# Kernel tuning notes

Measured on AMD Instinct MI355X. Metric: run time of the kernel, lower is better.

Reference implementation:

```python
import jax, jax.numpy as jnp
import numpy as np

SEQ_LEN = 2048
DIM = 1024
DIM_HEAD = 64
NHEAD = DIM // DIM_HEAD


def setup_inputs() -> dict:
    key = jax.random.key(0)
    k1, k2, k3 = jax.random.split(key, 3)
    x = jax.random.normal(k1, (SEQ_LEN, DIM), dtype=jnp.float32)
    # ortho_init approximated by scaled gaussian weights (same math path in forward)
    Wqkv = jax.random.normal(k2, (DIM, 3 * DIM), dtype=jnp.float32) / np.sqrt(DIM)
    Wout = jax.random.normal(k3, (DIM, DIM), dtype=jnp.float32) / np.sqrt(DIM)
    bias = jnp.zeros((DIM,), dtype=jnp.float32)
    return {"x": x, "Wqkv": Wqkv, "Wout": Wout, "bias": bias}


def reference(x, Wqkv, Wout, bias):
    seq_len = x.shape[-2]
    qkv = x @ Wqkv  # [S, 3*dim]
    qkv = jnp.reshape(qkv, (-1, 3, NHEAD, DIM_HEAD))  # [S,3,H,D]
    qkv = jnp.swapaxes(qkv, 0, 2)  # [H,3,S,D]
    q, k, v = (jax.lax.index_in_dim(qkv, i, -3, keepdims=False) for i in range(3))
    # [H,S,S] full logits, scaled
    logits = q @ jnp.swapaxes(k, -1, -2) / jnp.sqrt(DIM_HEAD)
    mask = jnp.tril(jnp.ones((seq_len, seq_len), dtype=jnp.float32))
    logits = jnp.where(mask, logits, jnp.finfo(logits.dtype).min)
    dtype = logits.dtype
    probs = jax.nn.softmax(logits.astype(jnp.float32), axis=-1).astype(dtype)
    attn_outs = probs @ v  # [H,S,D]
    attn_outs = jnp.reshape(jnp.swapaxes(attn_outs, 0, 1), (-1, NHEAD * DIM_HEAD))
    return attn_outs @ Wout + bias
```

## Files before the change

kernel.cpp:

```cpp
#include <hip/hip_runtime.h>
#include <cstdint>

#define SEQ_LEN 2048
#define DIM 1024
#define NHEAD 16
#define DHEAD 64
#define QKV_LD (3 * DIM)

typedef unsigned short u16;
typedef short bf16x8 __attribute__((ext_vector_type(8)));
typedef float f32x4 __attribute__((ext_vector_type(4)));

__device__ __forceinline__ u16 f2bf(float f) {
    union { float f; unsigned u; } v;
    v.f = f;
    unsigned r = v.u + 0x7fff + ((v.u >> 16) & 1);
    return (u16)(r >> 16);
}

__device__ __forceinline__ void load_lds16(const void* g, void* l) {
    __builtin_amdgcn_global_load_lds(
        (const __attribute__((address_space(1))) void*)g,
        (__attribute__((address_space(3))) void*)l, 16, 0, 0);
}

__device__ __forceinline__ void transpose_tile(const float* __restrict__ W,
                                               u16* __restrict__ Wt, int K, int N,
                                               int bx, int by, int t, float (*tile)[33]) {
    const int n0 = bx * 32, k0 = by * 32;
    const int tx = t & 31, ty = t >> 5;
#pragma unroll
    for (int i = 0; i < 32; i += 8)
        tile[ty + i][tx] = W[(size_t)(k0 + ty + i) * N + n0 + tx];
    __syncthreads();
#pragma unroll
    for (int i = 0; i < 32; i += 8)
        Wt[(size_t)(n0 + ty + i) * K + k0 + tx] = f2bf(tile[tx][ty + i]);
}

__global__ __launch_bounds__(256) void prep_k(const float* __restrict__ x,
                                              const float* __restrict__ Wqkv,
                                              const float* __restrict__ Wout,
                                              u16* __restrict__ xb,
                                              u16* __restrict__ Wqkvt,
                                              u16* __restrict__ Woutt) {
    __shared__ float tile[32][33];
    const int b = blockIdx.x;
    const int t = threadIdx.x;
    if (b < 2048) {
        const int i = b * 256 + t;
        const float4 v = reinterpret_cast<const float4*>(x)[i];
        const unsigned p0 = (unsigned)f2bf(v.x) | ((unsigned)f2bf(v.y) << 16);
        const unsigned p1 = (unsigned)f2bf(v.z) | ((unsigned)f2bf(v.w) << 16);
        reinterpret_cast<uint2*>(xb)[i] = make_uint2(p0, p1);
    } else if (b < 5120) {
        const int b2 = b - 2048;
        transpose_tile(Wqkv, Wqkvt, DIM, QKV_LD, b2 % 96, b2 / 96, t, tile);
    } else {
        const int b3 = b - 5120;
        transpose_tile(Wout, Woutt, DIM, DIM, b3 & 31, b3 >> 5, t, tile);
    }
}

template <int MODE, int BM, int BN, int BK>
__global__ __launch_bounds__(256) void gemm_bf16(const u16* __restrict__ A,
                                                 const u16* __restrict__ Bt,
                                                 const float* __restrict__ bias,
                                                 void* __restrict__ Cout,
                                                 int M, int N, int K) {
    constexpr int AI = BM / 32;
    constexpr int BJ = BN / 32;
    constexpr int ASZ = BM * BK;
    constexpr int BSZ = BN * BK;
    __shared__ u16 As[2 * ASZ];
    __shared__ u16 Bs[2 * BSZ];

    const int t = threadIdx.x;
    const int lane = t & 63;
    const int quad = lane >> 4;
    const int l15 = lane & 15;
    const int w = t >> 6;
    const int wm = (w & 1) * (BM / 2);
    const int wn = (w >> 1) * (BN / 2);
    const int m0 = blockIdx.y * BM;
    const int n0 = blockIdx.x * BN;
    const int sr = t >> 2;
    const int sc = (t & 3) << 3;

    const u16* Ab = A + (size_t)(m0 + sr) * K + sc;
    const u16* Bb = Bt + (size_t)(n0 + sr) * K + sc;

    auto stage = [&](int buf, int k0) {
#pragma unroll
        for (int kc = 0; kc < BK / 32; ++kc) {
#pragma unroll
            for (int c = 0; c < BM / 64; ++c)
                load_lds16(Ab + (size_t)(c * 64) * K + k0 + kc * 32,
                           &As[buf * ASZ + kc * BM * 32 + c * 2048 + t * 8]);
#pragma unroll
            for (int c = 0; c < BN / 64; ++c)
                load_lds16(Bb + (size_t)(c * 64) * K + k0 + kc * 32,
                           &Bs[buf * BSZ + kc * BN * 32 + c * 2048 + t * 8]);
        }
    };

    stage(0, 0);
    f32x4 acc[AI][BJ] = {};

    const int niter = K / BK;
    for (int it = 0; it < niter; ++it) {
        const int cur = it & 1, nxt = cur ^ 1;
        __syncthreads();
        if (it + 1 < niter) stage(nxt, (it + 1) * BK);
#pragma unroll
        for (int kc = 0; kc < BK / 32; ++kc) {
            bf16x8 af[AI], bfr[BJ];
#pragma unroll
            for (int i = 0; i < AI; ++i)
                af[i] = *reinterpret_cast<const bf16x8*>(
                    &As[cur * ASZ + kc * BM * 32 + (wm + i * 16 + l15) * 32 + quad * 8]);
#pragma unroll
            for (int j = 0; j < BJ; ++j)
                bfr[j] = *reinterpret_cast<const bf16x8*>(
                    &Bs[cur * BSZ + kc * BN * 32 + (wn + j * 16 + l15) * 32 + quad * 8]);
#pragma unroll
            for (int i = 0; i < AI; ++i)
#pragma unroll
                for (int j = 0; j < BJ; ++j)
                    acc[i][j] =
                        __builtin_amdgcn_mfma_f32_16x16x32_bf16(af[i], bfr[j], acc[i][j], 0, 0, 0);
        }
    }

#pragma unroll
    for (int j = 0; j < BJ; ++j) {
        const int col = n0 + wn + j * 16 + l15;
        float bv = 0.f;
        if constexpr (MODE == 1) bv = bias[col];
#pragma unroll
        for (int i = 0; i < AI; ++i) {
            const int row = m0 + wm + i * 16 + quad * 4;
#pragma unroll
            for (int r = 0; r < 4; ++r) {
                const float v = acc[i][j][r];
                if constexpr (MODE == 1)
                    ((float*)Cout)[(size_t)(row + r) * N + col] = v + bv;
                else
                    ((u16*)Cout)[(size_t)(row + r) * N + col] = f2bf(v);
            }
        }
    }
}

__global__ __launch_bounds__(256) void attn_mfma(const u16* __restrict__ qkv,
                                                 u16* __restrict__ O) {
    constexpr int PSTR = 40;
    __shared__ u16 SM[2560 + 4096 + 4096];
    u16* Ps = SM;
    u16* Ks = SM + 2560;
    u16* Vt = SM + 2560 + 4096;
    float* Ored = (float*)SM;
    float* Lred = Ored + 32 * 66;

    const int b = blockIdx.x;
    const int i = 63 - (b >> 4);
    const int h = b & 15;
    const int q0 = i * 32;
    const int jmax = i >> 1;

    const int t = threadIdx.x;
    const int lane = t & 63;
    const int quad = lane >> 4;
    const int l15 = lane & 15;
    const int w = t >> 6;
    const int wq = w >> 1;
    const int wk = w & 1;

    const int sr = t >> 2;
    const int sc = (t & 3) << 3;
    const int vp = (t & 31) * 2;
    const int vq = (t >> 5) * 8;

    load_lds16(qkv + (size_t)(q0 + ((t >> 2) & 31)) * QKV_LD + h * DHEAD + (t >> 7) * 32 + sc,
               &SM[t * 8]);
    const u16* kp0 = qkv + (size_t)sr * QKV_LD + DIM + h * DHEAD + sc;
    uint4 ka = *reinterpret_cast<const uint4*>(kp0);
    uint4 kb = *reinterpret_cast<const uint4*>(kp0 + 32);
    const u16* vp0 = qkv + (size_t)vp * QKV_LD + 2 * DIM + h * DHEAD + vq;
    uint4 va = *reinterpret_cast<const uint4*>(vp0);
    uint4 vb = *reinterpret_cast<const uint4*>(vp0 + QKV_LD);

    __syncthreads();
    const bf16x8 qf0 = *reinterpret_cast<const bf16x8*>(&SM[(wq * 16 + l15) * 32 + quad * 8]);
    const bf16x8 qf1 =
        *reinterpret_cast<const bf16x8*>(&SM[1024 + (wq * 16 + l15) * 32 + quad * 8]);
    __syncthreads();

    auto writeKV = [&](const uint4& kA, const uint4& kB, const uint4& vA, const uint4& vB) {
        *reinterpret_cast<uint4*>(&Ks[t * 8]) = kA;
        *reinterpret_cast<uint4*>(&Ks[2048 + t * 8]) = kB;
        const unsigned a4[4] = {vA.x, vA.y, vA.z, vA.w};
        const unsigned b4[4] = {vB.x, vB.y, vB.z, vB.w};
#pragma unroll
        for (int idx = 0; idx < 8; ++idx) {
            const unsigned lo = (idx & 1) ? (a4[idx >> 1] >> 16) : (a4[idx >> 1] & 0xffffu);
            const unsigned hi = (idx & 1) ? (b4[idx >> 1] >> 16) : (b4[idx >> 1] & 0xffffu);
            const int d = vq + idx;
            const int pos = d * 64 + (((vp >> 3) ^ (d & 7)) << 3) + (vp & 7);
            *reinterpret_cast<unsigned*>(&Vt[pos]) = lo | (hi << 16);
        }
    };
    writeKV(ka, kb, va, vb);
    __syncthreads();

    f32x4 oacc[4] = {};
    float lsum[4] = {0.f, 0.f, 0.f, 0.f};
    u16* Pw = Ps + w * 16 * PSTR;
    const int rowl_base = (i & 1) * 32 + wq * 16 + quad * 4;
    constexpr float SCL = 0.18033688f;

    for (int jt = 0; jt <= jmax; ++jt) {
        if (jt < jmax) {
            const int j1 = (jt + 1) * 64;
            const u16* kp = qkv + (size_t)(j1 + sr) * QKV_LD + DIM + h * DHEAD + sc;
            ka = *reinterpret_cast<const uint4*>(kp);
            kb = *reinterpret_cast<const uint4*>(kp + 32);
            const u16* vpt = qkv + (size_t)(j1 + vp) * QKV_LD + 2 * DIM + h * DHEAD + vq;
            va = *reinterpret_cast<const uint4*>(vpt);
            vb = *reinterpret_cast<const uint4*>(vpt + QKV_LD);
        }

        f32x4 sacc[2] = {};
#pragma unroll
        for (int nn = 0; nn < 2; ++nn) {
            const int krow = (wk * 32 + nn * 16 + l15) * 32 + quad * 8;
            const bf16x8 kf0 = *reinterpret_cast<const bf16x8*>(&Ks[krow]);
            sacc[nn] = __builtin_amdgcn_mfma_f32_16x16x32_bf16(qf0, kf0, sacc[nn], 0, 0, 0);
            const bf16x8 kf1 = *reinterpret_cast<const bf16x8*>(&Ks[2048 + krow]);
            sacc[nn] = __builtin_amdgcn_mfma_f32_16x16x32_bf16(qf1, kf1, sacc[nn], 0, 0, 0);
        }

        const bool diag = (jt == jmax);
#pragma unroll
        for (int r = 0; r < 4; ++r) {
            float p0 = sacc[0][r] * SCL, p1 = sacc[1][r] * SCL;
            if (diag) {
                const int rowl = rowl_base + r;
                if (wk * 32 + l15 > rowl) p0 = -1e30f;
                if (wk * 32 + 16 + l15 > rowl) p1 = -1e30f;
            }
            p0 = exp2f(p0);
            p1 = exp2f(p1);
            lsum[r] += p0 + p1;
            Pw[(quad * 4 + r) * PSTR + l15] = (u16)(__float_as_uint(p0) >> 16);
            Pw[(quad * 4 + r) * PSTR + 16 + l15] = (u16)(__float_as_uint(p1) >> 16);
        }

        const bf16x8 pf = *reinterpret_cast<const bf16x8*>(&Pw[l15 * PSTR + quad * 8]);
#pragma unroll
        for (int nd = 0; nd < 4; ++nd) {
            const int dloc = nd * 16 + l15;
            const bf16x8 vf = *reinterpret_cast<const bf16x8*>(
                &Vt[dloc * 64 + (((wk * 4 + quad) ^ (dloc & 7)) << 3)]);
            oacc[nd] = __builtin_amdgcn_mfma_f32_16x16x32_bf16(pf, vf, oacc[nd], 0, 0, 0);
        }

        if (jt < jmax) {
            __syncthreads();
            writeKV(ka, kb, va, vb);
            __syncthreads();
        }
    }

#pragma unroll
    for (int r = 0; r < 4; ++r) {
        float l = lsum[r];
#pragma unroll
        for (int off = 1; off < 16; off <<= 1) l += __shfl_xor(l, off, 64);
        lsum[r] = l;
    }
    __syncthreads();
    if (l15 == 0)
#pragma unroll
        for (int r = 0; r < 4; ++r) Lred[wk * 32 + wq * 16 + quad * 4 + r] = lsum[r];
    if (wk == 1)
#pragma unroll
        for (int nd = 0; nd < 4; ++nd)
#pragma unroll
            for (int r = 0; r < 4; ++r)
                Ored[(wq * 16 + quad * 4 + r) * 66 + nd * 16 + l15] = oacc[nd][r];
    __syncthreads();
    if (wk == 0) {
        float inv[4];
#pragma unroll
        for (int r = 0; r < 4; ++r) {
            const int rr = wq * 16 + quad * 4 + r;
            inv[r] = 1.0f / (Lred[rr] + Lred[32 + rr]);
        }
#pragma unroll
        for (int nd = 0; nd < 4; ++nd)
#pragma unroll
            for (int r = 0; r < 4; ++r) {
                const int rr = wq * 16 + quad * 4 + r;
                O[(size_t)(q0 + rr) * DIM + h * DHEAD + nd * 16 + l15] =
                    f2bf((oacc[nd][r] + Ored[rr * 66 + nd * 16 + l15]) * inv[r]);
            }
    }
}

extern "C" void kernel_launch(void* const* d_in, const int* in_sizes, int n_in,
                              void* d_out, int out_size, void* d_ws, size_t ws_size,
                              hipStream_t stream) {
    const float* x = (const float*)d_in[0];
    const float* Wqkv = (const float*)d_in[1];
    const float* Wout = (const float*)d_in[2];
    const float* bias = (const float*)d_in[3];
    float* out = (float*)d_out;

    char* ws = (char*)d_ws;
    u16* xb = (u16*)ws;
    u16* Wqkvt = (u16*)(ws + (4u << 20));
    u16* Woutt = (u16*)(ws + (10u << 20));
    u16* qkvb = (u16*)(ws + (12u << 20));
    u16* Ob = (u16*)(ws + (24u << 20));

    prep_k<<<dim3(6144), 256, 0, stream>>>(x, Wqkv, Wout, xb, Wqkvt, Woutt);

    gemm_bf16<0, 128, 64, 32><<<dim3(QKV_LD / 64, SEQ_LEN / 128), 256, 0, stream>>>(
        xb, Wqkvt, nullptr, qkvb, SEQ_LEN, QKV_LD, DIM);

    attn_mfma<<<dim3(64 * NHEAD), 256, 0, stream>>>(qkvb, Ob);

    gemm_bf16<1, 64, 64, 64><<<dim3(DIM / 64, SEQ_LEN / 64), 256, 0, stream>>>(
        Ob, Woutt, bias, out, SEQ_LEN, DIM, DIM);
}
```

Measured before the change: 151.6 us.

## Split causal attention over key chunks with a separate partial-sum reduction kernel

The single attention kernel becomes two kernels. The first processes at most four 64-key tiles per block, spread over a second grid dimension, and writes unnormalized fp32 partial outputs and row sums to workspace. The second kernel adds up the chunks, normalizes, and writes the bf16 output. This is meant to remove the causal load imbalance, where late query tiles looped over up to 32 key tiles, and to expose more parallel blocks. The cost is extra fp32 partial traffic to global memory, one more launch, and many blocks that exit early.

```diff
diff --git a/kernel.cpp b/kernel.cpp
--- a/kernel.cpp
+++ b/kernel.cpp
@@ -152,8 +152,9 @@
     }
 }
 
-__global__ __launch_bounds__(256) void attn_mfma(const u16* __restrict__ qkv,
-                                                 u16* __restrict__ O) {
+__global__ __launch_bounds__(256) void attn_part(const u16* __restrict__ qkv,
+                                                 float* __restrict__ Opart,
+                                                 float* __restrict__ Lpart) {
     constexpr int PSTR = 40;
     __shared__ u16 SM[2560 + 4096 + 4096];
     u16* Ps = SM;
@@ -162,11 +163,15 @@
     float* Ored = (float*)SM;
     float* Lred = Ored + 32 * 66;
 
-    const int b = blockIdx.x;
-    const int i = 63 - (b >> 4);
-    const int h = b & 15;
+    const int ih = blockIdx.x;
+    const int i = ih >> 4;
+    const int h = ih & 15;
+    const int c = blockIdx.y;
+    if (c > (i >> 3)) return;
     const int q0 = i * 32;
     const int jmax = i >> 1;
+    const int jlo = c * 4;
+    const int jhi = min(jlo + 3, jmax);
 
     const int t = threadIdx.x;
     const int lane = t & 63;
@@ -183,10 +188,10 @@
 
     load_lds16(qkv + (size_t)(q0 + ((t >> 2) & 31)) * QKV_LD + h * DHEAD + (t >> 7) * 32 + sc,
                &SM[t * 8]);
-    const u16* kp0 = qkv + (size_t)sr * QKV_LD + DIM + h * DHEAD + sc;
+    const u16* kp0 = qkv + (size_t)(jlo * 64 + sr) * QKV_LD + DIM + h * DHEAD + sc;
     uint4 ka = *reinterpret_cast<const uint4*>(kp0);
     uint4 kb = *reinterpret_cast<const uint4*>(kp0 + 32);
-    const u16* vp0 = qkv + (size_t)vp * QKV_LD + 2 * DIM + h * DHEAD + vq;
+    const u16* vp0 = qkv + (size_t)(jlo * 64 + vp) * QKV_LD + 2 * DIM + h * DHEAD + vq;
     uint4 va = *reinterpret_cast<const uint4*>(vp0);
     uint4 vb = *reinterpret_cast<const uint4*>(vp0 + QKV_LD);
 
@@ -219,8 +224,8 @@
     const int rowl_base = (i & 1) * 32 + wq * 16 + quad * 4;
     constexpr float SCL = 0.18033688f;
 
-    for (int jt = 0; jt <= jmax; ++jt) {
-        if (jt < jmax) {
+    for (int jt = jlo; jt <= jhi; ++jt) {
+        if (jt < jhi) {
             const int j1 = (jt + 1) * 64;
             const u16* kp = qkv + (size_t)(j1 + sr) * QKV_LD + DIM + h * DHEAD + sc;
             ka = *reinterpret_cast<const uint4*>(kp);
@@ -265,7 +270,7 @@
             oacc[nd] = __builtin_amdgcn_mfma_f32_16x16x32_bf16(pf, vf, oacc[nd], 0, 0, 0);
         }
 
-        if (jt < jmax) {
+        if (jt < jhi) {
             __syncthreads();
             writeKV(ka, kb, va, vb);
             __syncthreads();
@@ -291,21 +296,50 @@
                 Ored[(wq * 16 + quad * 4 + r) * 66 + nd * 16 + l15] = oacc[nd][r];
     __syncthreads();
     if (wk == 0) {
-        float inv[4];
+        const size_t pbase = ((size_t)ih * 8 + c) * 32;
 #pragma unroll
         for (int r = 0; r < 4; ++r) {
             const int rr = wq * 16 + quad * 4 + r;
-            inv[r] = 1.0f / (Lred[rr] + Lred[32 + rr]);
+            if (l15 == 0) Lpart[pbase + rr] = Lred[rr] + Lred[32 + rr];
         }
 #pragma unroll
         for (int nd = 0; nd < 4; ++nd)
 #pragma unroll
             for (int r = 0; r < 4; ++r) {
                 const int rr = wq * 16 + quad * 4 + r;
-                O[(size_t)(q0 + rr) * DIM + h * DHEAD + nd * 16 + l15] =
-                    f2bf((oacc[nd][r] + Ored[rr * 66 + nd * 16 + l15]) * inv[r]);
+                Opart[(pbase + rr) * 64 + nd * 16 + l15] =
+                    oacc[nd][r] + Ored[rr * 66 + nd * 16 + l15];
             }
     }
+}
+
+__global__ __launch_bounds__(256) void attn_reduce(const float* __restrict__ Opart,
+                                                   const float* __restrict__ Lpart,
+                                                   u16* __restrict__ O) {
+    const int ih = blockIdx.x;
+    const int i = ih >> 4, h = ih & 15;
+    const int nc = (i >> 3) + 1;
+    const int t = threadIdx.x;
+    const int r = t >> 3;
+    const int dg = (t & 7) * 8;
+
+    float acc[8] = {};
+    float l = 0.f;
+    for (int c = 0; c < nc; ++c) {
+        const size_t pbase = ((size_t)ih * 8 + c) * 32 + r;
+        const float4 a = *reinterpret_cast<const float4*>(&Opart[pbase * 64 + dg]);
+        const float4 b = *reinterpret_cast<const float4*>(&Opart[pbase * 64 + dg + 4]);
+        acc[0] += a.x; acc[1] += a.y; acc[2] += a.z; acc[3] += a.w;
+        acc[4] += b.x; acc[5] += b.y; acc[6] += b.z; acc[7] += b.w;
+        l += Lpart[pbase];
+    }
+    const float inv = 1.0f / l;
+    unsigned pk[4];
+#pragma unroll
+    for (int e = 0; e < 4; ++e)
+        pk[e] = (unsigned)f2bf(acc[2 * e] * inv) | ((unsigned)f2bf(acc[2 * e + 1] * inv) << 16);
+    *reinterpret_cast<uint4*>(&O[(size_t)(i * 32 + r) * DIM + h * DHEAD + dg]) =
+        make_uint4(pk[0], pk[1], pk[2], pk[3]);
 }
 
 extern "C" void kernel_launch(void* const* d_in, const int* in_sizes, int n_in,
@@ -323,13 +357,16 @@
     u16* Woutt = (u16*)(ws + (10u << 20));
     u16* qkvb = (u16*)(ws + (12u << 20));
     u16* Ob = (u16*)(ws + (24u << 20));
+    float* Opart = (float*)(ws + (32ull << 20));
+    float* Lpart = (float*)(ws + (100ull << 20));
 
     prep_k<<<dim3(6144), 256, 0, stream>>>(x, Wqkv, Wout, xb, Wqkvt, Woutt);
 
     gemm_bf16<0, 128, 64, 32><<<dim3(QKV_LD / 64, SEQ_LEN / 128), 256, 0, stream>>>(
         xb, Wqkvt, nullptr, qkvb, SEQ_LEN, QKV_LD, DIM);
 
-    attn_mfma<<<dim3(64 * NHEAD), 256, 0, stream>>>(qkvb, Ob);
+    attn_part<<<dim3(64 * NHEAD, 8), 256, 0, stream>>>(qkvb, Opart, Lpart);
+    attn_reduce<<<dim3(64 * NHEAD), 256, 0, stream>>>(Opart, Lpart, Ob);
 
     gemm_bf16<1, 64, 64, 64><<<dim3(DIM / 64, SEQ_LEN / 64), 256, 0, stream>>>(
         Ob, Woutt, bias, out, SEQ_LEN, DIM, DIM);
```

Measured after the change: 158.4 us. 1.05x slower.

## Emit pre-swizzled K and transposed V from QKV GEMM; 64-row attention tiles with async LDS staging

Applied to the files above, without the earlier changes.

The QKV GEMM epilogue now writes Q, K and V into separate buffers. K is stored with an XOR swizzle and V is stored transposed and swizzled per head, so the attention kernel can stage them straight into LDS with global_load_lds double buffering. Previously it loaded into registers, did a scalar transpose of V, and wrote LDS with two barriers per tile. The attention tile grows from 32 to 64 query rows per block, which halves the block count and reuses each K/V tile for twice as many queries. In exchange, the GEMM does strided scattered stores, LDS use per block goes up, and fewer blocks means less parallelism and coarser causal load balance.

```diff
diff --git a/kernel.cpp b/kernel.cpp
--- a/kernel.cpp
+++ b/kernel.cpp
@@ -67,6 +67,8 @@
                                                  const u16* __restrict__ Bt,
                                                  const float* __restrict__ bias,
                                                  void* __restrict__ Cout,
+                                                 u16* __restrict__ kout,
+                                                 u16* __restrict__ vout,
                                                  int M, int N, int K) {
     constexpr int AI = BM / 32;
     constexpr int BJ = BN / 32;
@@ -132,41 +134,87 @@
         }
     }
 
-#pragma unroll
-    for (int j = 0; j < BJ; ++j) {
-        const int col = n0 + wn + j * 16 + l15;
-        float bv = 0.f;
-        if constexpr (MODE == 1) bv = bias[col];
-#pragma unroll
-        for (int i = 0; i < AI; ++i) {
-            const int row = m0 + wm + i * 16 + quad * 4;
-#pragma unroll
-            for (int r = 0; r < 4; ++r) {
-                const float v = acc[i][j][r];
-                if constexpr (MODE == 1)
-                    ((float*)Cout)[(size_t)(row + r) * N + col] = v + bv;
-                else
-                    ((u16*)Cout)[(size_t)(row + r) * N + col] = f2bf(v);
-            }
-        }
-    }
-}
-
-__global__ __launch_bounds__(256) void attn_mfma(const u16* __restrict__ qkv,
+    if constexpr (MODE == 1) {
+#pragma unroll
+        for (int j = 0; j < BJ; ++j) {
+            const int col = n0 + wn + j * 16 + l15;
+            const float bv = bias[col];
+#pragma unroll
+            for (int i = 0; i < AI; ++i) {
+                const int row = m0 + wm + i * 16 + quad * 4;
+#pragma unroll
+                for (int r = 0; r < 4; ++r)
+                    ((float*)Cout)[(size_t)(row + r) * N + col] = acc[i][j][r] + bv;
+            }
+        }
+    } else {
+        const int region = n0 >> 10;
+        if (region == 0) {
+#pragma unroll
+            for (int j = 0; j < BJ; ++j) {
+                const int col = n0 + wn + j * 16 + l15;
+#pragma unroll
+                for (int i = 0; i < AI; ++i) {
+                    const int row = m0 + wm + i * 16 + quad * 4;
+#pragma unroll
+                    for (int r = 0; r < 4; ++r)
+                        ((u16*)Cout)[(size_t)(row + r) * DIM + col] = f2bf(acc[i][j][r]);
+                }
+            }
+        } else if (region == 1) {
+#pragma unroll
+            for (int j = 0; j < BJ; ++j) {
+                const int hd = n0 + wn + j * 16 + l15 - 1024;
+                const int d = hd & 63, hb = hd & ~63;
+#pragma unroll
+                for (int i = 0; i < AI; ++i) {
+                    const int row = m0 + wm + i * 16 + quad * 4;
+#pragma unroll
+                    for (int r = 0; r < 4; ++r) {
+                        const int s = row + r;
+                        const int pos = hb + ((((d >> 3) ^ (s & 7)) << 3) | (d & 7));
+                        kout[(size_t)s * DIM + pos] = f2bf(acc[i][j][r]);
+                    }
+                }
+            }
+        } else {
+#pragma unroll
+            for (int j = 0; j < BJ; ++j) {
+                const int hd = n0 + wn + j * 16 + l15 - 2048;
+#pragma unroll
+                for (int i = 0; i < AI; ++i) {
+                    const int srow = m0 + wm + i * 16 + quad * 4;
+                    const unsigned p0 = (unsigned)f2bf(acc[i][j][0]) |
+                                        ((unsigned)f2bf(acc[i][j][1]) << 16);
+                    const unsigned p1 = (unsigned)f2bf(acc[i][j][2]) |
+                                        ((unsigned)f2bf(acc[i][j][3]) << 16);
+                    const int pos = (srow & ~63) + ((((srow >> 3) & 7) ^ (hd & 7)) << 3) +
+                                    (srow & 7);
+                    *reinterpret_cast<uint2*>(&vout[(size_t)hd * SEQ_LEN + pos]) =
+                        make_uint2(p0, p1);
+                }
+            }
+        }
+    }
+}
+
+__global__ __launch_bounds__(256) void attn_mfma(const u16* __restrict__ Qb,
+                                                 const u16* __restrict__ Kb,
+                                                 const u16* __restrict__ Vg,
                                                  u16* __restrict__ O) {
     constexpr int PSTR = 40;
-    __shared__ u16 SM[2560 + 4096 + 4096];
-    u16* Ps = SM;
-    u16* Ks = SM + 2560;
-    u16* Vt = SM + 2560 + 4096;
-    float* Ored = (float*)SM;
-    float* Lred = Ored + 32 * 66;
+    __shared__ u16 SM[4096 + 8192 + 8192 + 4 * 32 * PSTR];
+    u16* Qs = SM;
+    u16* Ks = SM + 4096;
+    u16* Vs = SM + 4096 + 8192;
+    u16* Ps = SM + 4096 + 16384;
+    float* OredF = (float*)SM;
+    float* LredF = (float*)(SM + 4096 + 8192 + 4096);
 
     const int b = blockIdx.x;
-    const int i = 63 - (b >> 4);
+    const int qt = 31 - (b >> 4);
     const int h = b & 15;
-    const int q0 = i * 32;
-    const int jmax = i >> 1;
+    const int q0 = qt * 64;
 
     const int t = threadIdx.x;
     const int lane = t & 63;
@@ -176,134 +224,134 @@
     const int wq = w >> 1;
     const int wk = w & 1;
 
-    const int sr = t >> 2;
-    const int sc = (t & 3) << 3;
-    const int vp = (t & 31) * 2;
-    const int vq = (t >> 5) * 8;
-
-    load_lds16(qkv + (size_t)(q0 + ((t >> 2) & 31)) * QKV_LD + h * DHEAD + (t >> 7) * 32 + sc,
-               &SM[t * 8]);
-    const u16* kp0 = qkv + (size_t)sr * QKV_LD + DIM + h * DHEAD + sc;
-    uint4 ka = *reinterpret_cast<const uint4*>(kp0);
-    uint4 kb = *reinterpret_cast<const uint4*>(kp0 + 32);
-    const u16* vp0 = qkv + (size_t)vp * QKV_LD + 2 * DIM + h * DHEAD + vq;
-    uint4 va = *reinterpret_cast<const uint4*>(vp0);
-    uint4 vb = *reinterpret_cast<const uint4*>(vp0 + QKV_LD);
-
+    const int drow = t >> 3;
+    const int doff = (t & 7) * 8;
+
+    auto stageK = [&](int buf, int j0) {
+#pragma unroll
+        for (int c = 0; c < 2; ++c)
+            load_lds16(Kb + (size_t)(j0 + c * 32 + (drow & 31)) * DIM + h * DHEAD + doff,
+                       &Ks[buf * 4096 + c * 2048 + t * 8]);
+    };
+    auto stageV = [&](int buf, int j0) {
+#pragma unroll
+        for (int c = 0; c < 2; ++c)
+            load_lds16(Vg + (size_t)(h * DHEAD + c * 32 + (drow & 31)) * SEQ_LEN + j0 + doff,
+                       &Vs[buf * 4096 + c * 2048 + t * 8]);
+    };
+
+#pragma unroll
+    for (int c = 0; c < 2; ++c)
+        load_lds16(Qb + (size_t)(q0 + c * 32 + (drow & 31)) * DIM + h * DHEAD + doff,
+                   &Qs[c * 2048 + t * 8]);
+    stageK(0, 0);
+    stageV(0, 0);
     __syncthreads();
-    const bf16x8 qf0 = *reinterpret_cast<const bf16x8*>(&SM[(wq * 16 + l15) * 32 + quad * 8]);
-    const bf16x8 qf1 =
-        *reinterpret_cast<const bf16x8*>(&SM[1024 + (wq * 16 + l15) * 32 + quad * 8]);
+
+    bf16x8 qf[2][2];
+#pragma unroll
+    for (int qq = 0; qq < 2; ++qq)
+#pragma unroll
+        for (int dc = 0; dc < 2; ++dc)
+            qf[qq][dc] = *reinterpret_cast<const bf16x8*>(
+                &Qs[(wq * 32 + qq * 16 + l15) * 64 + dc * 32 + quad * 8]);
+
+    f32x4 oacc[2][4] = {};
+    float lsum[2][4] = {};
+    u16* Pw = Ps + w * 32 * PSTR;
+    constexpr float SCL = 0.18033688f;
+
+    for (int jt = 0; jt <= qt; ++jt) {
+        const int cur = jt & 1, nxt = cur ^ 1;
+        if (jt > 0) __syncthreads();
+        if (jt < qt) {
+            stageK(nxt, (jt + 1) * 64);
+            stageV(nxt, (jt + 1) * 64);
+        }
+
+        f32x4 sacc[2][2] = {};
+#pragma unroll
+        for (int nn = 0; nn < 2; ++nn)
+#pragma unroll
+            for (int dc = 0; dc < 2; ++dc) {
+                const bf16x8 kf = *reinterpret_cast<const bf16x8*>(
+                    &Ks[cur * 4096 + (wk * 32 + nn * 16 + l15) * 64 +
+                        (((dc * 4 + quad) ^ (l15 & 7)) << 3)]);
+#pragma unroll
+                for (int qq = 0; qq < 2; ++qq)
+                    sacc[qq][nn] =
+                        __builtin_amdgcn_mfma_f32_16x16x32_bf16(qf[qq][dc], kf, sacc[qq][nn], 0, 0, 0);
+            }
+
+        const bool diag = (jt == qt);
+#pragma unroll
+        for (int qq = 0; qq < 2; ++qq)
+#pragma unroll
+            for (int r = 0; r < 4; ++r) {
+                const int rowl = wq * 32 + qq * 16 + quad * 4 + r;
+                float p0 = sacc[qq][0][r] * SCL, p1 = sacc[qq][1][r] * SCL;
+                if (diag) {
+                    if (wk * 32 + l15 > rowl) p0 = -1e30f;
+                    if (wk * 32 + 16 + l15 > rowl) p1 = -1e30f;
+                }
+                p0 = exp2f(p0);
+                p1 = exp2f(p1);
+                lsum[qq][r] += p0 + p1;
+                const int pr = (qq * 16 + quad * 4 + r) * PSTR;
+                Pw[pr + l15] = (u16)(__float_as_uint(p0) >> 16);
+                Pw[pr + 16 + l15] = (u16)(__float_as_uint(p1) >> 16);
+            }
+
+#pragma unroll
+        for (int qq = 0; qq < 2; ++qq) {
+            const bf16x8 pf =
+                *reinterpret_cast<const bf16x8*>(&Pw[(qq * 16 + l15) * PSTR + quad * 8]);
+#pragma unroll
+            for (int nd = 0; nd < 4; ++nd) {
+                const bf16x8 vf = *reinterpret_cast<const bf16x8*>(
+                    &Vs[cur * 4096 + (nd * 16 + l15) * 64 +
+                        (((wk * 4 + quad) ^ (l15 & 7)) << 3)]);
+                oacc[qq][nd] =
+                    __builtin_amdgcn_mfma_f32_16x16x32_bf16(pf, vf, oacc[qq][nd], 0, 0, 0);
+            }
+        }
+    }
+
+#pragma unroll
+    for (int qq = 0; qq < 2; ++qq)
+#pragma unroll
+        for (int r = 0; r < 4; ++r) {
+            float l = lsum[qq][r];
+#pragma unroll
+            for (int off = 1; off < 16; off <<= 1) l += __shfl_xor(l, off, 64);
+            lsum[qq][r] = l;
+        }
     __syncthreads();
-
-    auto writeKV = [&](const uint4& kA, const uint4& kB, const uint4& vA, const uint4& vB) {
-        *reinterpret_cast<uint4*>(&Ks[t * 8]) = kA;
-        *reinterpret_cast<uint4*>(&Ks[2048 + t * 8]) = kB;
-        const unsigned a4[4] = {vA.x, vA.y, vA.z, vA.w};
-        const unsigned b4[4] = {vB.x, vB.y, vB.z, vB.w};
-#pragma unroll
-        for (int idx = 0; idx < 8; ++idx) {
-            const unsigned lo = (idx & 1) ? (a4[idx >> 1] >> 16) : (a4[idx >> 1] & 0xffffu);
-            const unsigned hi = (idx & 1) ? (b4[idx >> 1] >> 16) : (b4[idx >> 1] & 0xffffu);
-            const int d = vq + idx;
-            const int pos = d * 64 + (((vp >> 3) ^ (d & 7)) << 3) + (vp & 7);
-            *reinterpret_cast<unsigned*>(&Vt[pos]) = lo | (hi << 16);
-        }
-    };
-    writeKV(ka, kb, va, vb);
-    __syncthreads();
-
-    f32x4 oacc[4] = {};
-    float lsum[4] = {0.f, 0.f, 0.f, 0.f};
-    u16* Pw = Ps + w * 16 * PSTR;
-    const int rowl_base = (i & 1) * 32 + wq * 16 + quad * 4;
-    constexpr float SCL = 0.18033688f;
-
-    for (int jt = 0; jt <= jmax; ++jt) {
-        if (jt < jmax) {
-            const int j1 = (jt + 1) * 64;
-            const u16* kp = qkv + (size_t)(j1 + sr) * QKV_LD + DIM + h * DHEAD + sc;
-            ka = *reinterpret_cast<const uint4*>(kp);
-            kb = *reinterpret_cast<const uint4*>(kp + 32);
-            const u16* vpt = qkv + (size_t)(j1 + vp) * QKV_LD + 2 * DIM + h * DHEAD + vq;
-            va = *reinterpret_cast<const uint4*>(vpt);
-            vb = *reinterpret_cast<const uint4*>(vpt + QKV_LD);
-        }
-
-        f32x4 sacc[2] = {};
-#pragma unroll
-        for (int nn = 0; nn < 2; ++nn) {
-            const int krow = (wk * 32 + nn * 16 + l15) * 32 + quad * 8;
-            const bf16x8 kf0 = *reinterpret_cast<const bf16x8*>(&Ks[krow]);
-            sacc[nn] = __builtin_amdgcn_mfma_f32_16x16x32_bf16(qf0, kf0, sacc[nn], 0, 0, 0);
-            const bf16x8 kf1 = *reinterpret_cast<const bf16x8*>(&Ks[2048 + krow]);
-            sacc[nn] = __builtin_amdgcn_mfma_f32_16x16x32_bf16(qf1, kf1, sacc[nn], 0, 0, 0);
-        }
-
-        const bool diag = (jt == jmax);
-#pragma unroll
-        for (int r = 0; r < 4; ++r) {
-            float p0 = sacc[0][r] * SCL, p1 = sacc[1][r] * SCL;
-            if (diag) {
-                const int rowl = rowl_base + r;
-                if (wk * 32 + l15 > rowl) p0 = -1e30f;
-                if (wk * 32 + 16 + l15 > rowl) p1 = -1e30f;
-            }
-            p0 = exp2f(p0);
-            p1 = exp2f(p1);
-            lsum[r] += p0 + p1;
-            Pw[(quad * 4 + r) * PSTR + l15] = (u16)(__float_as_uint(p0) >> 16);
-            Pw[(quad * 4 + r) * PSTR + 16 + l15] = (u16)(__float_as_uint(p1) >> 16);
-        }
-
-        const bf16x8 pf = *reinterpret_cast<const bf16x8*>(&Pw[l15 * PSTR + quad * 8]);
-#pragma unroll
-        for (int nd = 0; nd < 4; ++nd) {
-            const int dloc = nd * 16 + l15;
-            const bf16x8 vf = *reinterpret_cast<const bf16x8*>(
-                &Vt[dloc * 64 + (((wk * 4 + quad) ^ (dloc & 7)) << 3)]);
-            oacc[nd] = __builtin_amdgcn_mfma_f32_16x16x32_bf16(pf, vf, oacc[nd], 0, 0, 0);
-        }
-
-        if (jt < jmax) {
-            __syncthreads();
-            writeKV(ka, kb, va, vb);
-            __syncthreads();
-        }
-    }
-
-#pragma unroll
-    for (int r = 0; r < 4; ++r) {
-        float l = lsum[r];
-#pragma unroll
-        for (int off = 1; off < 16; off <<= 1) l += __shfl_xor(l, off, 64);
-        lsum[r] = l;
-    }
-    __syncthreads();
-    if (l15 == 0)
-#pragma unroll
-        for (int r = 0; r < 4; ++r) Lred[wk * 32 + wq * 16 + quad * 4 + r] = lsum[r];
-    if (wk == 1)
-#pragma unroll
-        for (int nd = 0; nd < 4; ++nd)
-#pragma unroll
-            for (int r = 0; r < 4; ++r)
-                Ored[(wq * 16 + quad * 4 + r) * 66 + nd * 16 + l15] = oacc[nd][r];
+    if (wk == 1) {
+#pragma unroll
+        for (int qq = 0; qq < 2; ++qq)
+#pragma unroll
+            for (int r = 0; r < 4; ++r) {
+                const int rowl = wq * 32 + qq * 16 + quad * 4 + r;
+                if (l15 == 0) LredF[rowl] = lsum[qq][r];
+#pragma unroll
+                for (int nd = 0; nd < 4; ++nd)
+                    OredF[rowl * 68 + nd * 16 + l15] = oacc[qq][nd][r];
+            }
+    }
     __syncthreads();
     if (wk == 0) {
-        float inv[4];
-#pragma unroll
-        for (int r = 0; r < 4; ++r) {
-            const int rr = wq * 16 + quad * 4 + r;
-            inv[r] = 1.0f / (Lred[rr] + Lred[32 + rr]);
-        }
-#pragma unroll
-        for (int nd = 0; nd < 4; ++nd)
+#pragma unroll
+        for (int qq = 0; qq < 2; ++qq)
 #pragma unroll
             for (int r = 0; r < 4; ++r) {
-                const int rr = wq * 16 + quad * 4 + r;
-                O[(size_t)(q0 + rr) * DIM + h * DHEAD + nd * 16 + l15] =
-                    f2bf((oacc[nd][r] + Ored[rr * 66 + nd * 16 + l15]) * inv[r]);
+                const int rowl = wq * 32 + qq * 16 + quad * 4 + r;
+                const float inv = 1.0f / (lsum[qq][r] + LredF[rowl]);
+                const int row = q0 + rowl;
+#pragma unroll
+                for (int nd = 0; nd < 4; ++nd)
+                    O[(size_t)row * DIM + h * DHEAD + nd * 16 + l15] =
+                        f2bf((oacc[qq][nd][r] + OredF[rowl * 68 + nd * 16 + l15]) * inv);
             }
     }
 }
@@ -321,16 +369,18 @@
     u16* xb = (u16*)ws;
     u16* Wqkvt = (u16*)(ws + (4u << 20));
     u16* Woutt = (u16*)(ws + (10u << 20));
-    u16* qkvb = (u16*)(ws + (12u << 20));
+    u16* Qb = (u16*)(ws + (12u << 20));
+    u16* Kb = (u16*)(ws + (16u << 20));
+    u16* Vg = (u16*)(ws + (20u << 20));
     u16* Ob = (u16*)(ws + (24u << 20));
 
     prep_k<<<dim3(6144), 256, 0, stream>>>(x, Wqkv, Wout, xb, Wqkvt, Woutt);
 
     gemm_bf16<0, 128, 64, 32><<<dim3(QKV_LD / 64, SEQ_LEN / 128), 256, 0, stream>>>(
-        xb, Wqkvt, nullptr, qkvb, SEQ_LEN, QKV_LD, DIM);
-
-    attn_mfma<<<dim3(64 * NHEAD), 256, 0, stream>>>(qkvb, Ob);
+        xb, Wqkvt, nullptr, Qb, Kb, Vg, SEQ_LEN, QKV_LD, DIM);
+
+    attn_mfma<<<dim3(32 * NHEAD), 256, 0, stream>>>(Qb, Kb, Vg, Ob);
 
     gemm_bf16<1, 64, 64, 64><<<dim3(DIM / 64, SEQ_LEN / 64), 256, 0, stream>>>(
-        Ob, Woutt, bias, out, SEQ_LEN, DIM, DIM);
-}
+        Ob, Woutt, bias, out, nullptr, nullptr, SEQ_LEN, DIM, DIM);
+}
```

After: 146.8 us. 1.03x faster.
